# Optimization experiments

Hardware: AMD Instinct MI355X
Metric: run time of the kernel (lower is better)

Reference implementation:

```python
import jax, jax.numpy as jnp
import numpy as np

NUM_HEADS = 16
HEAD_DIM = 64
HIDDEN = NUM_HEADS * HEAD_DIM  # 1024


def get_rel_pos(q_size, k_size, rel_pos):
    # q_size == k_size here and rel_pos already has 2*size-1 rows, so the
    # F.interpolate(mode='linear') resize in the original is an identity.
    # relative_coords = q - k + (k_size - 1)  (scale factors are 1.0)
    coords = jnp.arange(q_size)[:, None] - jnp.arange(k_size)[None, :] + (k_size - 1)
    return rel_pos[coords]  # [q_size, k_size, head_dim]


def setup_inputs() -> dict:
    key = jax.random.key(0)
    ks = jax.random.split(key, 7)
    B, H, W = 4, 56, 28
    inp = {
        "hidden_states": jax.random.normal(ks[0], (B, H, W, HIDDEN), jnp.float32),
        "qkv_w": jax.random.normal(ks[1], (3 * HIDDEN, HIDDEN), jnp.float32) * 0.02,
        "qkv_b": jax.random.normal(ks[2], (3 * HIDDEN,), jnp.float32) * 0.02,
        "proj_w": jax.random.normal(ks[3], (HIDDEN, HIDDEN), jnp.float32) * 0.02,
        "proj_b": jax.random.normal(ks[4], (HIDDEN,), jnp.float32) * 0.02,
        "rel_pos_h": jax.random.normal(ks[5], (2 * H - 1, HEAD_DIM), jnp.float32) * 0.02,
        "rel_pos_w": jax.random.normal(ks[6], (2 * W - 1, HEAD_DIM), jnp.float32) * 0.02,
    }
    return inp


def reference(hidden_states, qkv_w, qkv_b, proj_w, proj_b, rel_pos_h, rel_pos_w):
    B, H, W, C = hidden_states.shape
    N = H * W
    scale = HEAD_DIM ** -0.5

    # qkv projection -> [3, B*heads, N, head_dim]
    qkv = hidden_states @ qkv_w.T + qkv_b
    qkv = qkv.reshape(B, N, 3, NUM_HEADS, HEAD_DIM).transpose(2, 0, 3, 1, 4)
    qkv = qkv.reshape(3, B * NUM_HEADS, N, HEAD_DIM)
    query, key_, value = qkv[0], qkv[1], qkv[2]

    # scaled dot-product scores, fully materialized as in the original
    attn = jnp.einsum('bqd,bkd->bqk', query * scale, key_)  # [B*heads, N, N]

    # decomposed relative position bias
    Rh = get_rel_pos(H, H, rel_pos_h)  # [H, H, d]
    Rw = get_rel_pos(W, W, rel_pos_w)  # [W, W, d]
    q_r = query.reshape(B * NUM_HEADS, H, W, HEAD_DIM)
    rel_h = jnp.einsum('bhwc,hkc->bhwk', q_r, Rh)  # [B*heads, H, W, H]
    rel_w = jnp.einsum('bhwc,wkc->bhwk', q_r, Rw)  # [B*heads, H, W, W]
    attn = attn.reshape(B * NUM_HEADS, H, W, H, W)
    attn = attn + rel_h[:, :, :, :, None] + rel_w[:, :, :, None, :]
    attn = attn.reshape(B * NUM_HEADS, N, N)

    attn = jax.nn.softmax(attn.astype(jnp.float32), axis=-1).astype(query.dtype)

    out = jnp.einsum('bqk,bkd->bqd', attn, value)
    out = out.reshape(B, NUM_HEADS, H, W, HEAD_DIM).transpose(0, 2, 3, 1, 4)
    out = out.reshape(B, H, W, C)
    out = out @ proj_w.T + proj_b
    return out
```

## Files before the change

### kernel.cpp

```cpp
#include <hip/hip_runtime.h>
#include <hip/hip_bf16.h>
#include <stdint.h>

typedef __bf16 bf16;
typedef __bf16 bf16x2 __attribute__((ext_vector_type(2)));
typedef __bf16 bf16x4 __attribute__((ext_vector_type(4)));
typedef __bf16 bf16x8 __attribute__((ext_vector_type(8)));
typedef float f32x4 __attribute__((ext_vector_type(4)));

#define AS1 __attribute__((address_space(1)))
#define AS3 __attribute__((address_space(3)))

static __device__ __forceinline__ float b2f(bf16 x) { return (float)x; }

static __device__ __forceinline__ void async_cp16(const bf16* g, bf16* l) {
    __builtin_amdgcn_global_load_lds((const AS1 void*)g, (AS3 void*)l, 16, 0, 0);
}

static __device__ __forceinline__ bf16x4 cvt4(f32x4 v) {
    bf16x4 r;
    r[0] = (bf16)v[0]; r[1] = (bf16)v[1]; r[2] = (bf16)v[2]; r[3] = (bf16)v[3];
    return r;
}

static __device__ __forceinline__ float fast_exp2(float x) {
#if __has_builtin(__builtin_amdgcn_exp2f)
    return __builtin_amdgcn_exp2f(x);
#else
    return __expf(x * 0.69314718056f);
#endif
}

__global__ __launch_bounds__(256) void cvt_kernel(
    const float* __restrict__ src, bf16* __restrict__ dst, int n4) {
    int i = blockIdx.x * 256 + threadIdx.x;
    const int stride = gridDim.x * 256;
    for (; i < n4; i += stride)
        ((bf16x4*)dst)[i] = cvt4(((const f32x4*)src)[i]);
}


#define QKV_EPILOGUE()                                                        \
    for (int nt = 0; nt < 4; nt++) {                                          \
        const int n_ = n0 + wn + nt * 16 + lm;                                \
        const float bv = bias[n_];                                            \
        const int s = n_ >> 10, rem = n_ & 1023;                              \
        const int h = rem >> 6, d = rem & 63;                                 \
        for (int mt = 0; mt < 4; mt++) {                                      \
            for (int r = 0; r < 4; r++) {                                     \
                const int m_ = m0 + wm + mt * 16 + quad * 4 + r;              \
                const int b = m_ / 1568;                                      \
                const int pix = m_ - b * 1568;                                \
                const int g = b * 16 + h;                                     \
                const bf16 v = (bf16)(acc[mt][nt][r] + bv);                   \
                if (s == 0)      Qb[((size_t)g * 1568 + pix) * 64 + d] = v;   \
                else if (s == 1) Kb[((size_t)g * 1568 + pix) * 64 + d] = v;   \
                else {                                                        \
                    const int lk = pix & 31;                                  \
                    const int ppix = (pix & ~31) | ((lk & 15) << 1) | (lk >> 4); \
                    Vt[((size_t)g * 64 + d) * 1568 + ppix] = v;               \
                }                                                             \
            }                                                                 \
        }                                                                     \
    }

__global__ __launch_bounds__(256) void qkv_gemm_bf16(
    const bf16* __restrict__ A, const bf16* __restrict__ W,
    const float* __restrict__ bias, bf16* __restrict__ Qb,
    bf16* __restrict__ Kb, bf16* __restrict__ Vt) {
    __shared__ bf16 As[128 * 32];
    __shared__ bf16 Bs[128 * 32];
    const int t = threadIdx.x;
    const int wid = t >> 6, lane = t & 63;
    const int m0 = blockIdx.x * 128, n0 = blockIdx.y * 128;
    const int wm = (wid & 1) * 64, wn = (wid >> 1) * 64;
    const int r_i = lane >> 2, c8 = (lane & 3) * 8;
    const int lm = lane & 15, quad = lane >> 4;

    f32x4 acc[4][4] = {};
    for (int k0 = 0; k0 < 1024; k0 += 32) {
        __syncthreads();
        for (int i = 0; i < 2; i++) {
            const int blk = wid * 2 + i;
            async_cp16(A + (size_t)(m0 + blk * 16 + r_i) * 1024 + k0 + c8, As + blk * 512);
            async_cp16(W + (size_t)(n0 + blk * 16 + r_i) * 1024 + k0 + c8, Bs + blk * 512);
        }
        __syncthreads();
        bf16x8 af[4], bfr[4];
        for (int x = 0; x < 4; x++) {
            af[x]  = *(const bf16x8*)&As[(wm + x * 16 + lm) * 32 + quad * 8];
            bfr[x] = *(const bf16x8*)&Bs[(wn + x * 16 + lm) * 32 + quad * 8];
        }
        for (int mt = 0; mt < 4; mt++)
            for (int nt = 0; nt < 4; nt++)
                acc[mt][nt] = __builtin_amdgcn_mfma_f32_16x16x32_bf16(af[mt], bfr[nt], acc[mt][nt], 0, 0, 0);
    }
    QKV_EPILOGUE()
}

__global__ __launch_bounds__(256) void qkv_gemm_f32(
    const float* __restrict__ A, const float* __restrict__ W,
    const float* __restrict__ bias, bf16* __restrict__ Qb,
    bf16* __restrict__ Kb, bf16* __restrict__ Vt) {
    __shared__ bf16 As[128 * 32];
    __shared__ bf16 Bs[128 * 32];
    const int t = threadIdx.x;
    const int wid = t >> 6, lane = t & 63;
    const int m0 = blockIdx.x * 128, n0 = blockIdx.y * 128;
    const int wm = (wid & 1) * 64, wn = (wid >> 1) * 64;
    const int lm = lane & 15, quad = lane >> 4;

    f32x4 acc[4][4] = {};
    for (int k0 = 0; k0 < 1024; k0 += 32) {
        __syncthreads();
        for (int i = 0; i < 4; i++) {
            const int idx = t + i * 256;
            const int row = idx >> 3, c4 = (idx & 7) * 4;
            const f32x4 av = *(const f32x4*)&A[(size_t)(m0 + row) * 1024 + k0 + c4];
            const f32x4 wv = *(const f32x4*)&W[(size_t)(n0 + row) * 1024 + k0 + c4];
            *(bf16x4*)&As[row * 32 + c4] = cvt4(av);
            *(bf16x4*)&Bs[row * 32 + c4] = cvt4(wv);
        }
        __syncthreads();
        bf16x8 af[4], bfr[4];
        for (int x = 0; x < 4; x++) {
            af[x]  = *(const bf16x8*)&As[(wm + x * 16 + lm) * 32 + quad * 8];
            bfr[x] = *(const bf16x8*)&Bs[(wn + x * 16 + lm) * 32 + quad * 8];
        }
        for (int mt = 0; mt < 4; mt++)
            for (int nt = 0; nt < 4; nt++)
                acc[mt][nt] = __builtin_amdgcn_mfma_f32_16x16x32_bf16(af[mt], bfr[nt], acc[mt][nt], 0, 0, 0);
    }
    QKV_EPILOGUE()
}

__global__ __launch_bounds__(256) void flash_attn(
    const bf16* __restrict__ Qb, const bf16* __restrict__ Kb,
    const bf16* __restrict__ Vt, const float* __restrict__ rph,
    const float* __restrict__ rpw, bf16* __restrict__ AO) {
    const int x = blockIdx.x;
    const int xcd = x & 7, j = x >> 3;
    const int g = xcd * 8 + j / 25;
    const int qblk = j - (j / 25) * 25;
    const int q0 = qblk * 64;

    __shared__ __align__(16) char smem[38400];
    bf16* Th  = (bf16*)smem;
    bf16* Tw  = (bf16*)(smem + 14592);
    char* B   = smem + 22016;
    bf16* Qs  = (bf16*)B;
    bf16* RPs = (bf16*)B;
    bf16* Ks  = (bf16*)B;
    bf16* Vts = (bf16*)(B + 4608);
    bf16* Ps  = (bf16*)(B + 9728);

    const int t = threadIdx.x, wid = t >> 6, lane = t & 63;
    const int lm = lane & 15, quad = lane >> 4;
    const int qbase_l = wid * 16 + quad * 4;

    for (int c = t; c < 512; c += 256) {
        const int row = c >> 3, col = (c & 7) * 8;
        const int qg = min(q0 + row, 1567);
        *(bf16x8*)&Qs[row * 72 + col] =
            *(const bf16x8*)&Qb[((size_t)g * 1568 + qg) * 64 + col];
    }
    __syncthreads();
    const int qrow_l = wid * 16 + lm;
    const bf16x8 qf0 = *(const bf16x8*)&Qs[qrow_l * 72 + quad * 8];
    const bf16x8 qf1 = *(const bf16x8*)&Qs[qrow_l * 72 + 32 + quad * 8];
    int thb[4], twb[4];
#pragma unroll
    for (int r = 0; r < 4; r++) {
        const int qg = min(q0 + qbase_l + r, 1567);
        const int hq = qg / 28;
        thb[r] = (qbase_l + r) * 114 + hq + 55;
        twb[r] = (qbase_l + r) * 58 + (qg - hq * 28) + 27;
    }
    __syncthreads();

    for (int c = t; c < 1776; c += 256) {
        const int row = c >> 4, col = (c & 15) * 4;
        *(bf16x4*)&RPs[row * 72 + col] = cvt4(*(const f32x4*)&rph[row * 64 + col]);
    }
    __syncthreads();
    f32x4 acch[7];
#pragma unroll
    for (int nt = 0; nt < 7; nt++) {
        const bf16x8 b0 = *(const bf16x8*)&RPs[(nt * 16 + lm) * 72 + quad * 8];
        const bf16x8 b1 = *(const bf16x8*)&RPs[(nt * 16 + lm) * 72 + 32 + quad * 8];
        f32x4 a = {};
        a = __builtin_amdgcn_mfma_f32_16x16x32_bf16(qf0, b0, a, 0, 0, 0);
        a = __builtin_amdgcn_mfma_f32_16x16x32_bf16(qf1, b1, a, 0, 0, 0);
        acch[nt] = a;
    }
    __syncthreads();

    for (int c = t; c < 880; c += 256) {
        const int row = c >> 4, col = (c & 15) * 4;
        *(bf16x4*)&RPs[row * 72 + col] = cvt4(*(const f32x4*)&rpw[row * 64 + col]);
    }
#pragma unroll
    for (int nt = 0; nt < 7; nt++)
#pragma unroll
        for (int r = 0; r < 4; r++)
            Th[(qbase_l + r) * 114 + nt * 16 + lm] = (bf16)(acch[nt][r] * 8.0f);
    __syncthreads();
#pragma unroll
    for (int nt = 0; nt < 4; nt++) {
        const bf16x8 b0 = *(const bf16x8*)&RPs[(nt * 16 + lm) * 72 + quad * 8];
        const bf16x8 b1 = *(const bf16x8*)&RPs[(nt * 16 + lm) * 72 + 32 + quad * 8];
        f32x4 a = {};
        a = __builtin_amdgcn_mfma_f32_16x16x32_bf16(qf0, b0, a, 0, 0, 0);
        a = __builtin_amdgcn_mfma_f32_16x16x32_bf16(qf1, b1, a, 0, 0, 0);
        const int col = nt * 16 + lm;
        if (col < 58) {
#pragma unroll
            for (int r = 0; r < 4; r++)
                Tw[(qbase_l + r) * 58 + col] = (bf16)(a[r] * 8.0f);
        }
    }

    f32x4 o[4] = {};
    float l_lane[4] = {0.f, 0.f, 0.f, 0.f};
    const float C2 = 0.125f * 1.44269504f;
    const float S2 = 10.0f * 1.44269504f;

    const int ks_k = t >> 3, ks_d = (t & 7) * 8;
    const int vs_d = t >> 2, vs_k = (t & 3) * 8;
    bf16* Pw = &Ps[wid * 640];

    int hk0 = 0, wk0 = lm;
    int hk1 = (16 + lm) >= 28 ? 1 : 0;
    int wk1 = 16 + lm - (hk1 ? 28 : 0);

    const size_t kgbase = ((size_t)g * 1568 + ks_k) * 64 + ks_d;
    const size_t vgbase = ((size_t)g * 64 + vs_d) * 1568 + vs_k;
    bf16x8 kreg = *(const bf16x8*)&Kb[kgbase];
    bf16x8 vreg = *(const bf16x8*)&Vt[vgbase];

    for (int kt = 0; kt < 49; kt++) {
        f32x4 s0, s1;
#pragma unroll
        for (int r = 0; r < 4; r++) {
            s0[r] = b2f(Th[thb[r] - hk0]) + b2f(Tw[twb[r] - wk0]);
            s1[r] = b2f(Th[thb[r] - hk1]) + b2f(Tw[twb[r] - wk1]);
        }

        __syncthreads();
        *(bf16x8*)&Ks[ks_k * 72 + ks_d] = kreg;
        *(bf16x8*)&Vts[vs_d * 40 + vs_k] = vreg;
        {
            const int ktn = min(kt + 1, 48);
            kreg = *(const bf16x8*)&Kb[kgbase + (size_t)ktn * 2048];
            vreg = *(const bf16x8*)&Vt[vgbase + ktn * 32];
        }
        __syncthreads();

        {
            const bf16x8 ka0 = *(const bf16x8*)&Ks[lm * 72 + quad * 8];
            const bf16x8 ka1 = *(const bf16x8*)&Ks[lm * 72 + 32 + quad * 8];
            s0 = __builtin_amdgcn_mfma_f32_16x16x32_bf16(qf0, ka0, s0, 0, 0, 0);
            s0 = __builtin_amdgcn_mfma_f32_16x16x32_bf16(qf1, ka1, s0, 0, 0, 0);
            const bf16x8 kb0 = *(const bf16x8*)&Ks[(16 + lm) * 72 + quad * 8];
            const bf16x8 kb1 = *(const bf16x8*)&Ks[(16 + lm) * 72 + 32 + quad * 8];
            s1 = __builtin_amdgcn_mfma_f32_16x16x32_bf16(qf0, kb0, s1, 0, 0, 0);
            s1 = __builtin_amdgcn_mfma_f32_16x16x32_bf16(qf1, kb1, s1, 0, 0, 0);
        }

#pragma unroll
        for (int r = 0; r < 4; r++) {
            const float p0 = fast_exp2(fmaf(s0[r], C2, -S2));
            const float p1 = fast_exp2(fmaf(s1[r], C2, -S2));
            l_lane[r] += p0 + p1;
            bf16x2 pp; pp[0] = (bf16)p0; pp[1] = (bf16)p1;
            *(bf16x2*)&Pw[(quad * 4 + r) * 40 + lm * 2] = pp;
        }
        wk0 += 4; hk0 += 1; if (wk0 >= 28) { wk0 -= 28; hk0 += 1; }
        wk1 += 4; hk1 += 1; if (wk1 >= 28) { wk1 -= 28; hk1 += 1; }

        __asm__ volatile("s_waitcnt lgkmcnt(0)" ::: "memory");
        const bf16x8 pf = *(const bf16x8*)&Pw[lm * 40 + quad * 8];
#pragma unroll
        for (int dt = 0; dt < 4; dt++) {
            const bf16x8 vf = *(const bf16x8*)&Vts[(dt * 16 + lm) * 40 + quad * 8];
            o[dt] = __builtin_amdgcn_mfma_f32_16x16x32_bf16(pf, vf, o[dt], 0, 0, 0);
        }
    }

    const int qrow0 = q0 + qbase_l;
    if (q0 + wid * 16 < 1568) {
        const int bo = g >> 4, h = g & 15;
#pragma unroll
        for (int r = 0; r < 4; r++) {
            float ll = l_lane[r];
            for (int off = 1; off < 16; off <<= 1) ll += __shfl_xor(ll, off, 64);
            const float inv = 1.0f / ll;
            const size_t base = ((size_t)bo * 1568 + qrow0 + r) * 1024 + h * 64;
            for (int dt = 0; dt < 4; dt++)
                AO[base + dt * 16 + lm] = (bf16)(o[dt][r] * inv);
        }
    }
}

__global__ __launch_bounds__(256) void proj_gemm_bf16(
    const bf16* __restrict__ A, const bf16* __restrict__ W,
    const float* __restrict__ bias, float* __restrict__ out) {
    __shared__ bf16 As[128 * 32];
    __shared__ bf16 Bs[128 * 32];
    const int t = threadIdx.x;
    const int wid = t >> 6, lane = t & 63;
    const int m0 = blockIdx.x * 128, n0 = blockIdx.y * 128;
    const int wm = (wid & 1) * 64, wn = (wid >> 1) * 64;
    const int r_i = lane >> 2, c8 = (lane & 3) * 8;
    const int lm = lane & 15, quad = lane >> 4;

    f32x4 acc[4][4] = {};
    for (int k0 = 0; k0 < 1024; k0 += 32) {
        __syncthreads();
        for (int i = 0; i < 2; i++) {
            const int blk = wid * 2 + i;
            async_cp16(A + (size_t)(m0 + blk * 16 + r_i) * 1024 + k0 + c8, As + blk * 512);
            async_cp16(W + (size_t)(n0 + blk * 16 + r_i) * 1024 + k0 + c8, Bs + blk * 512);
        }
        __syncthreads();
        bf16x8 af[4], bfr[4];
        for (int x = 0; x < 4; x++) {
            af[x]  = *(const bf16x8*)&As[(wm + x * 16 + lm) * 32 + quad * 8];
            bfr[x] = *(const bf16x8*)&Bs[(wn + x * 16 + lm) * 32 + quad * 8];
        }
        for (int mt = 0; mt < 4; mt++)
            for (int nt = 0; nt < 4; nt++)
                acc[mt][nt] = __builtin_amdgcn_mfma_f32_16x16x32_bf16(af[mt], bfr[nt], acc[mt][nt], 0, 0, 0);
    }
    for (int nt = 0; nt < 4; nt++) {
        const int n_ = n0 + wn + nt * 16 + lm;
        const float bv = bias[n_];
        for (int mt = 0; mt < 4; mt++)
            for (int r = 0; r < 4; r++) {
                const int m_ = m0 + wm + mt * 16 + quad * 4 + r;
                out[(size_t)m_ * 1024 + n_] = acc[mt][nt][r] + bv;
            }
    }
}

__global__ __launch_bounds__(256) void proj_gemm_f32(
    const bf16* __restrict__ A, const float* __restrict__ W,
    const float* __restrict__ bias, float* __restrict__ out) {
    __shared__ bf16 As[128 * 32];
    __shared__ bf16 Bs[128 * 32];
    const int t = threadIdx.x;
    const int wid = t >> 6, lane = t & 63;
    const int m0 = blockIdx.x * 128, n0 = blockIdx.y * 128;
    const int wm = (wid & 1) * 64, wn = (wid >> 1) * 64;
    const int r_i = lane >> 2, c8 = (lane & 3) * 8;
    const int lm = lane & 15, quad = lane >> 4;

    f32x4 acc[4][4] = {};
    for (int k0 = 0; k0 < 1024; k0 += 32) {
        __syncthreads();
        for (int i = 0; i < 2; i++) {
            const int blk = wid * 2 + i;
            async_cp16(A + (size_t)(m0 + blk * 16 + r_i) * 1024 + k0 + c8, As + blk * 512);
        }
        for (int i = 0; i < 4; i++) {
            const int idx = t + i * 256;
            const int row = idx >> 3, c4 = (idx & 7) * 4;
            const f32x4 wv = *(const f32x4*)&W[(size_t)(n0 + row) * 1024 + k0 + c4];
            *(bf16x4*)&Bs[row * 32 + c4] = cvt4(wv);
        }
        __syncthreads();
        bf16x8 af[4], bfr[4];
        for (int x = 0; x < 4; x++) {
            af[x]  = *(const bf16x8*)&As[(wm + x * 16 + lm) * 32 + quad * 8];
            bfr[x] = *(const bf16x8*)&Bs[(wn + x * 16 + lm) * 32 + quad * 8];
        }
        for (int mt = 0; mt < 4; mt++)
            for (int nt = 0; nt < 4; nt++)
                acc[mt][nt] = __builtin_amdgcn_mfma_f32_16x16x32_bf16(af[mt], bfr[nt], acc[mt][nt], 0, 0, 0);
    }
    for (int nt = 0; nt < 4; nt++) {
        const int n_ = n0 + wn + nt * 16 + lm;
        const float bv = bias[n_];
        for (int mt = 0; mt < 4; mt++)
            for (int r = 0; r < 4; r++) {
                const int m_ = m0 + wm + mt * 16 + quad * 4 + r;
                out[(size_t)m_ * 1024 + n_] = acc[mt][nt][r] + bv;
            }
    }
}

extern "C" void kernel_launch(void* const* d_in, const int* in_sizes, int n_in,
                              void* d_out, int out_size, void* d_ws, size_t ws_size,
                              hipStream_t stream) {
    const float* hs     = (const float*)d_in[0];
    const float* qkv_w  = (const float*)d_in[1];
    const float* qkv_b  = (const float*)d_in[2];
    const float* proj_w = (const float*)d_in[3];
    const float* proj_b = (const float*)d_in[4];
    const float* rph    = (const float*)d_in[5];
    const float* rpw    = (const float*)d_in[6];
    float* out = (float*)d_out;

    const size_t GQ = (size_t)64 * 1568 * 64;
    const size_t N_HS = (size_t)6272 * 1024;
    const size_t N_QW = (size_t)3072 * 1024;
    const size_t N_PW = (size_t)1024 * 1024;
    bf16* Qb = (bf16*)d_ws;
    bf16* Kb = Qb + GQ;
    bf16* Vt = Kb + GQ;
    bf16* AO = Vt + GQ;
    bf16* hs_bf    = AO + GQ;
    bf16* qkvw_bf  = hs_bf + N_HS;
    bf16* projw_bf = qkvw_bf + N_QW;
    const size_t need = (4 * GQ + N_HS + N_QW + N_PW) * sizeof(bf16);

    if (ws_size >= need) {
        cvt_kernel<<<512, 256, 0, stream>>>(hs, hs_bf, (int)(N_HS / 4));
        cvt_kernel<<<512, 256, 0, stream>>>(qkv_w, qkvw_bf, (int)(N_QW / 4));
        cvt_kernel<<<256, 256, 0, stream>>>(proj_w, projw_bf, (int)(N_PW / 4));
        qkv_gemm_bf16<<<dim3(49, 24), 256, 0, stream>>>(hs_bf, qkvw_bf, qkv_b, Qb, Kb, Vt);
        flash_attn<<<1600, 256, 0, stream>>>(Qb, Kb, Vt, rph, rpw, AO);
        proj_gemm_bf16<<<dim3(49, 8), 256, 0, stream>>>(AO, projw_bf, proj_b, out);
    } else {
        qkv_gemm_f32<<<dim3(49, 24), 256, 0, stream>>>(hs, qkv_w, qkv_b, Qb, Kb, Vt);
        flash_attn<<<1600, 256, 0, stream>>>(Qb, Kb, Vt, rph, rpw, AO);
        proj_gemm_f32<<<dim3(49, 8), 256, 0, stream>>>(AO, proj_w, proj_b, out);
    }
}
```

Baseline: 348.1 us.

## Widen flash-attention key tiles to 64 with swizzled LDS and MFMA row sums

The attention loop now processes 64 keys per iteration (25 iterations instead of 49), staging K and V in XOR-swizzled LDS tiles to avoid bank conflicts. The softmax scale and log2e are folded into Q in the QKV epilogue, and the rel-pos bias tables are kept in fp32 with the softmax offset prefolded, so each score needs only an add and exp2. Only the relative-position rows needed by this query block are converted. Row sums are accumulated with an MFMA against a ones vector instead of per-lane adds and shuffles, and s_setprio raises priority around the MFMA bursts. The changes raise LDS use and register pressure. Padding the tail key tile with masked scores adds some edge-case complexity.

```diff
diff --git a/kernel.cpp b/kernel.cpp
--- a/kernel.cpp
+++ b/kernel.cpp
@@ -10,8 +10,6 @@
 
 #define AS1 __attribute__((address_space(1)))
 #define AS3 __attribute__((address_space(3)))
-
-static __device__ __forceinline__ float b2f(bf16 x) { return (float)x; }
 
 static __device__ __forceinline__ void async_cp16(const bf16* g, bf16* l) {
     __builtin_amdgcn_global_load_lds((const AS1 void*)g, (AS3 void*)l, 16, 0, 0);
@@ -46,13 +44,14 @@
         const float bv = bias[n_];                                            \
         const int s = n_ >> 10, rem = n_ & 1023;                              \
         const int h = rem >> 6, d = rem & 63;                                 \
+        const float qsc = (s == 0) ? 0.18033688011112042f : 1.0f;             \
         for (int mt = 0; mt < 4; mt++) {                                      \
             for (int r = 0; r < 4; r++) {                                     \
                 const int m_ = m0 + wm + mt * 16 + quad * 4 + r;              \
                 const int b = m_ / 1568;                                      \
                 const int pix = m_ - b * 1568;                                \
                 const int g = b * 16 + h;                                     \
-                const bf16 v = (bf16)(acc[mt][nt][r] + bv);                   \
+                const bf16 v = (bf16)((acc[mt][nt][r] + bv) * qsc);           \
                 if (s == 0)      Qb[((size_t)g * 1568 + pix) * 64 + d] = v;   \
                 else if (s == 1) Kb[((size_t)g * 1568 + pix) * 64 + d] = v;   \
                 else {                                                        \
@@ -143,20 +142,24 @@
     const int g = xcd * 8 + j / 25;
     const int qblk = j - (j / 25) * 25;
     const int q0 = qblk * 64;
-
-    __shared__ __align__(16) char smem[38400];
-    bf16* Th  = (bf16*)smem;
-    bf16* Tw  = (bf16*)(smem + 14592);
-    char* B   = smem + 22016;
+    const int hqb = q0 / 28;
+
+    __shared__ __align__(16) char smem[51712];
+    float* Th = (float*)smem;
+    float* Tw = (float*)(smem + 15360);
+    const char* ThC = (const char*)smem;
+    const char* TwC = (const char*)(smem + 15360);
+    char* B   = smem + 30208;
     bf16* Qs  = (bf16*)B;
     bf16* RPs = (bf16*)B;
-    bf16* Ks  = (bf16*)B;
-    bf16* Vts = (bf16*)(B + 4608);
-    bf16* Ps  = (bf16*)(B + 9728);
+    char* KsC = B;
+    char* VsC = B + 8192;
+    bf16* Ps  = (bf16*)(B + 16384);
 
     const int t = threadIdx.x, wid = t >> 6, lane = t & 63;
     const int lm = lane & 15, quad = lane >> 4;
     const int qbase_l = wid * 16 + quad * 4;
+    const int swz = (lm & 7) << 4;
 
     for (int c = t; c < 512; c += 256) {
         const int row = c >> 3, col = (c & 7) * 8;
@@ -168,24 +171,34 @@
     const int qrow_l = wid * 16 + lm;
     const bf16x8 qf0 = *(const bf16x8*)&Qs[qrow_l * 72 + quad * 8];
     const bf16x8 qf1 = *(const bf16x8*)&Qs[qrow_l * 72 + 32 + quad * 8];
-    int thb[4], twb[4];
+
+    int thbB[4], twbB[4];
 #pragma unroll
     for (int r = 0; r < 4; r++) {
         const int qg = min(q0 + qbase_l + r, 1567);
-        const int hq = qg / 28;
-        thb[r] = (qbase_l + r) * 114 + hq + 55;
-        twb[r] = (qbase_l + r) * 58 + (qg - hq * 28) + 27;
+        const int hq = qg / 28, wq = qg - hq * 28;
+        thbB[r] = ((qbase_l + r) * 60 + (hq - hqb) + 55) * 4;
+        twbB[r] = ((qbase_l + r) * 58 + wq + 27) * 4;
+    }
+
+    bf16x8 kreg[2], vreg[2];
+#pragma unroll
+    for (int i = 0; i < 2; i++) {
+        const int idx = (i << 8) + t;
+        kreg[i] = *(const bf16x8*)&Kb[((size_t)g * 1568 + (idx >> 3)) * 64 + ((idx & 7) << 3)];
+        vreg[i] = *(const bf16x8*)&Vt[((size_t)g * 64 + (idx >> 3)) * 1568 + ((idx & 7) << 3)];
     }
     __syncthreads();
 
-    for (int c = t; c < 1776; c += 256) {
+    for (int c = t; c < 1024; c += 256) {
         const int row = c >> 4, col = (c & 15) * 4;
-        *(bf16x4*)&RPs[row * 72 + col] = cvt4(*(const f32x4*)&rph[row * 64 + col]);
+        const int rg = min(hqb + row, 110);
+        *(bf16x4*)&RPs[row * 72 + col] = cvt4(*(const f32x4*)&rph[rg * 64 + col]);
     }
     __syncthreads();
-    f32x4 acch[7];
-#pragma unroll
-    for (int nt = 0; nt < 7; nt++) {
+    f32x4 acch[4];
+#pragma unroll
+    for (int nt = 0; nt < 4; nt++) {
         const bf16x8 b0 = *(const bf16x8*)&RPs[(nt * 16 + lm) * 72 + quad * 8];
         const bf16x8 b1 = *(const bf16x8*)&RPs[(nt * 16 + lm) * 72 + 32 + quad * 8];
         f32x4 a = {};
@@ -195,15 +208,20 @@
     }
     __syncthreads();
 
-    for (int c = t; c < 880; c += 256) {
+    for (int c = t; c < 1024; c += 256) {
         const int row = c >> 4, col = (c & 15) * 4;
-        *(bf16x4*)&RPs[row * 72 + col] = cvt4(*(const f32x4*)&rpw[row * 64 + col]);
-    }
-#pragma unroll
-    for (int nt = 0; nt < 7; nt++)
-#pragma unroll
-        for (int r = 0; r < 4; r++)
-            Th[(qbase_l + r) * 114 + nt * 16 + lm] = (bf16)(acch[nt][r] * 8.0f);
+        const int rg = min(row, 54);
+        *(bf16x4*)&RPs[row * 72 + col] = cvt4(*(const f32x4*)&rpw[rg * 64 + col]);
+    }
+#pragma unroll
+    for (int nt = 0; nt < 4; nt++) {
+        const int c = nt * 16 + lm;
+        if (c < 59) {
+#pragma unroll
+            for (int r = 0; r < 4; r++)
+                Th[(qbase_l + r) * 60 + c] = acch[nt][r] * 8.0f - 14.4269504f;
+        }
+    }
     __syncthreads();
 #pragma unroll
     for (int nt = 0; nt < 4; nt++) {
@@ -212,90 +230,123 @@
         f32x4 a = {};
         a = __builtin_amdgcn_mfma_f32_16x16x32_bf16(qf0, b0, a, 0, 0, 0);
         a = __builtin_amdgcn_mfma_f32_16x16x32_bf16(qf1, b1, a, 0, 0, 0);
-        const int col = nt * 16 + lm;
-        if (col < 58) {
+        const int c = nt * 16 + lm;
+        if (c < 55) {
 #pragma unroll
             for (int r = 0; r < 4; r++)
-                Tw[(qbase_l + r) * 58 + col] = (bf16)(a[r] * 8.0f);
+                Tw[(qbase_l + r) * 58 + c] = a[r] * 8.0f;
         }
     }
 
     f32x4 o[4] = {};
-    float l_lane[4] = {0.f, 0.f, 0.f, 0.f};
-    const float C2 = 0.125f * 1.44269504f;
-    const float S2 = 10.0f * 1.44269504f;
-
-    const int ks_k = t >> 3, ks_d = (t & 7) * 8;
-    const int vs_d = t >> 2, vs_k = (t & 3) * 8;
+    f32x4 lsum = {};
+    bf16x8 ones;
+#pragma unroll
+    for (int i = 0; i < 8; i++) ones[i] = (bf16)1.0f;
+
+    int hkB[4], wkB[4];
+#pragma unroll
+    for (int f = 0; f < 4; f++) {
+        const int k = f * 16 + lm;
+        const int hk = k / 28;
+        hkB[f] = hk * 4;
+        wkB[f] = (k - hk * 28) * 4;
+    }
     bf16* Pw = &Ps[wid * 640];
 
-    int hk0 = 0, wk0 = lm;
-    int hk1 = (16 + lm) >= 28 ? 1 : 0;
-    int wk1 = 16 + lm - (hk1 ? 28 : 0);
-
-    const size_t kgbase = ((size_t)g * 1568 + ks_k) * 64 + ks_d;
-    const size_t vgbase = ((size_t)g * 64 + vs_d) * 1568 + vs_k;
-    bf16x8 kreg = *(const bf16x8*)&Kb[kgbase];
-    bf16x8 vreg = *(const bf16x8*)&Vt[vgbase];
-
-    for (int kt = 0; kt < 49; kt++) {
-        f32x4 s0, s1;
+    for (int kt = 0; kt < 25; kt++) {
+        f32x4 s[4];
+#pragma unroll
+        for (int f = 0; f < 2; f++)
+#pragma unroll
+            for (int r = 0; r < 4; r++)
+                s[f][r] = *(const float*)(ThC + (thbB[r] - hkB[f]))
+                        + *(const float*)(TwC + (twbB[r] - wkB[f]));
+        if (kt < 24) {
+#pragma unroll
+            for (int f = 2; f < 4; f++)
+#pragma unroll
+                for (int r = 0; r < 4; r++)
+                    s[f][r] = *(const float*)(ThC + (thbB[r] - hkB[f]))
+                            + *(const float*)(TwC + (twbB[r] - wkB[f]));
+        } else {
+#pragma unroll
+            for (int f = 2; f < 4; f++)
+#pragma unroll
+                for (int r = 0; r < 4; r++)
+                    s[f][r] = -30000.0f;
+        }
+
+        __syncthreads();
+#pragma unroll
+        for (int i = 0; i < 2; i++) {
+            const int idx = (i << 8) + t;
+            const int row = idx >> 3;
+            const int cb = (((idx & 7) << 4) ^ ((row & 7) << 4));
+            *(bf16x8*)(KsC + row * 128 + cb) = kreg[i];
+            *(bf16x8*)(VsC + row * 128 + cb) = vreg[i];
+        }
+        {
+            const int kb = min(kt + 1, 24) << 6;
+#pragma unroll
+            for (int i = 0; i < 2; i++) {
+                const int idx = (i << 8) + t;
+                const int krow = min(kb + (idx >> 3), 1567);
+                kreg[i] = *(const bf16x8*)&Kb[((size_t)g * 1568 + krow) * 64 + ((idx & 7) << 3)];
+                const int vcol = min(kb + ((idx & 7) << 3), 1560);
+                vreg[i] = *(const bf16x8*)&Vt[((size_t)g * 64 + (idx >> 3)) * 1568 + vcol];
+            }
+        }
+        __syncthreads();
+
+        __builtin_amdgcn_s_setprio(1);
+#pragma unroll
+        for (int f = 0; f < 4; f++) {
+            const char* rp = KsC + (f * 16 + lm) * 128;
+            const int x0 = (quad * 16) ^ swz;
+            const bf16x8 ka = *(const bf16x8*)(rp + x0);
+            const bf16x8 kb2 = *(const bf16x8*)(rp + (x0 ^ 64));
+            s[f] = __builtin_amdgcn_mfma_f32_16x16x32_bf16(qf0, ka, s[f], 0, 0, 0);
+            s[f] = __builtin_amdgcn_mfma_f32_16x16x32_bf16(qf1, kb2, s[f], 0, 0, 0);
+        }
+        __builtin_amdgcn_s_setprio(0);
+
+#pragma unroll
+        for (int f = 0; f < 4; f++) {
+            wkB[f] += 32; hkB[f] += 8;
+            if (wkB[f] >= 112) { wkB[f] -= 112; hkB[f] += 4; }
+        }
+
+#pragma unroll
+        for (int h = 0; h < 2; h++) {
+#pragma unroll
+            for (int r = 0; r < 4; r++) {
+                const float p0 = fast_exp2(s[2 * h][r]);
+                const float p1 = fast_exp2(s[2 * h + 1][r]);
+                bf16x2 pp; pp[0] = (bf16)p0; pp[1] = (bf16)p1;
+                *(bf16x2*)&Pw[(quad * 4 + r) * 40 + lm * 2] = pp;
+            }
+            __asm__ volatile("s_waitcnt lgkmcnt(0)" ::: "memory");
+            const bf16x8 pf = *(const bf16x8*)&Pw[lm * 40 + quad * 8];
+            lsum = __builtin_amdgcn_mfma_f32_16x16x32_bf16(pf, ones, lsum, 0, 0, 0);
+            __builtin_amdgcn_s_setprio(1);
+#pragma unroll
+            for (int dt = 0; dt < 4; dt++) {
+                const bf16x8 vf = *(const bf16x8*)(VsC + (dt * 16 + lm) * 128 +
+                                                   (((h << 6) + quad * 16) ^ swz));
+                o[dt] = __builtin_amdgcn_mfma_f32_16x16x32_bf16(pf, vf, o[dt], 0, 0, 0);
+            }
+            __builtin_amdgcn_s_setprio(0);
+        }
+    }
+
+    if (q0 + wid * 16 < 1568) {
+        const int bo = g >> 4, hh = g & 15;
 #pragma unroll
         for (int r = 0; r < 4; r++) {
-            s0[r] = b2f(Th[thb[r] - hk0]) + b2f(Tw[twb[r] - wk0]);
-            s1[r] = b2f(Th[thb[r] - hk1]) + b2f(Tw[twb[r] - wk1]);
-        }
-
-        __syncthreads();
-        *(bf16x8*)&Ks[ks_k * 72 + ks_d] = kreg;
-        *(bf16x8*)&Vts[vs_d * 40 + vs_k] = vreg;
-        {
-            const int ktn = min(kt + 1, 48);
-            kreg = *(const bf16x8*)&Kb[kgbase + (size_t)ktn * 2048];
-            vreg = *(const bf16x8*)&Vt[vgbase + ktn * 32];
-        }
-        __syncthreads();
-
-        {
-            const bf16x8 ka0 = *(const bf16x8*)&Ks[lm * 72 + quad * 8];
-            const bf16x8 ka1 = *(const bf16x8*)&Ks[lm * 72 + 32 + quad * 8];
-            s0 = __builtin_amdgcn_mfma_f32_16x16x32_bf16(qf0, ka0, s0, 0, 0, 0);
-            s0 = __builtin_amdgcn_mfma_f32_16x16x32_bf16(qf1, ka1, s0, 0, 0, 0);
-            const bf16x8 kb0 = *(const bf16x8*)&Ks[(16 + lm) * 72 + quad * 8];
-            const bf16x8 kb1 = *(const bf16x8*)&Ks[(16 + lm) * 72 + 32 + quad * 8];
-            s1 = __builtin_amdgcn_mfma_f32_16x16x32_bf16(qf0, kb0, s1, 0, 0, 0);
-            s1 = __builtin_amdgcn_mfma_f32_16x16x32_bf16(qf1, kb1, s1, 0, 0, 0);
-        }
-
-#pragma unroll
-        for (int r = 0; r < 4; r++) {
-            const float p0 = fast_exp2(fmaf(s0[r], C2, -S2));
-            const float p1 = fast_exp2(fmaf(s1[r], C2, -S2));
-            l_lane[r] += p0 + p1;
-            bf16x2 pp; pp[0] = (bf16)p0; pp[1] = (bf16)p1;
-            *(bf16x2*)&Pw[(quad * 4 + r) * 40 + lm * 2] = pp;
-        }
-        wk0 += 4; hk0 += 1; if (wk0 >= 28) { wk0 -= 28; hk0 += 1; }
-        wk1 += 4; hk1 += 1; if (wk1 >= 28) { wk1 -= 28; hk1 += 1; }
-
-        __asm__ volatile("s_waitcnt lgkmcnt(0)" ::: "memory");
-        const bf16x8 pf = *(const bf16x8*)&Pw[lm * 40 + quad * 8];
-#pragma unroll
-        for (int dt = 0; dt < 4; dt++) {
-            const bf16x8 vf = *(const bf16x8*)&Vts[(dt * 16 + lm) * 40 + quad * 8];
-            o[dt] = __builtin_amdgcn_mfma_f32_16x16x32_bf16(pf, vf, o[dt], 0, 0, 0);
-        }
-    }
-
-    const int qrow0 = q0 + qbase_l;
-    if (q0 + wid * 16 < 1568) {
-        const int bo = g >> 4, h = g & 15;
-#pragma unroll
-        for (int r = 0; r < 4; r++) {
-            float ll = l_lane[r];
-            for (int off = 1; off < 16; off <<= 1) ll += __shfl_xor(ll, off, 64);
-            const float inv = 1.0f / ll;
-            const size_t base = ((size_t)bo * 1568 + qrow0 + r) * 1024 + h * 64;
+            const float inv = 1.0f / lsum[r];
+            const size_t base = ((size_t)bo * 1568 + q0 + qbase_l + r) * 1024 + hh * 64;
+#pragma unroll
             for (int dt = 0; dt < 4; dt++)
                 AO[base + dt * 16 + lm] = (bf16)(o[dt][r] * inv);
         }
```

New measurement: 337.9 us. 1.03x faster.
